# Kernel tuning notes

Measured on AMD Instinct MI355X. Metric: run time of the kernel, lower is better.

Reference implementation:

```python
import jax, jax.numpy as jnp
import numpy as np

NUM_LEAF = 10000   # leaf classes
BRANCH = 100       # leaves per parent node
NUM_PARENTS = NUM_LEAF // BRANCH  # 100 internal parent nodes (+ 1 implicit root)
BATCH = 4096


def setup_inputs() -> dict:
    key = jax.random.key(0)
    k1, k2 = jax.random.split(key)
    inp = jax.random.normal(k1, (BATCH, NUM_LEAF), dtype=jnp.float32)
    target = jax.random.randint(k2, (BATCH,), 0, NUM_LEAF)
    # structural tensor: parent id of each leaf in the 2-level taxonomy
    leaf_parent = (jnp.arange(NUM_LEAF) // BRANCH).astype(jnp.int32)
    return {"input": inp, "target": target, "leaf_parent": leaf_parent}


def _bce_to_one(p):
    # BCELoss(reduction='sum') against all-ones targets: -log(p), with torch's
    # log clamp at -100, after clipping p into [0, 1] as the module does.
    p = jnp.clip(p, 0.0, 1.0)
    return jnp.minimum(-jnp.log(p), 100.0)


def reference(input, target, leaf_parent):
    probs = jax.nn.softmax(input, axis=1)                       # [B, L]
    # mapping-sum for every internal parent node, all samples at once:
    # parent_probs[b, p] = sum_{l: parent(l)==p} probs[b, l]
    parent_probs = jax.ops.segment_sum(
        probs.T, leaf_parent, num_segments=NUM_PARENTS).T       # [B, P]
    b = jnp.arange(probs.shape[0])
    leaf_p = probs[b, target]                                   # group = leaf itself
    par_p = parent_probs[b, leaf_parent[target]]                # group = parent(leaf)
    root_p = probs.sum(axis=1)                                  # group = root (all leaves)
    per_sample = _bce_to_one(leaf_p) + _bce_to_one(par_p) + _bce_to_one(root_p)
    return per_sample.mean()  # reduction='mean'
```

## Files before the change

### kernel.cpp

```cpp
#include <hip/hip_runtime.h>


#define NUM_LEAF 10000
#define BRANCH   100
#define BATCH    4096
#define NV4      (NUM_LEAF / 4)

__global__ __launch_bounds__(256) void hce_row_kernel(
    const float* __restrict__ input,
    const int*   __restrict__ target,
    const int*   __restrict__ leaf_parent,
    float*       __restrict__ row_loss)
{
    const int row  = blockIdx.x;
    const int tid  = threadIdx.x;
    const int lane = tid & 63;
    const int wave = tid >> 6;

    const float*  x  = input + (size_t)row * NUM_LEAF;
    const float4* x4 = (const float4*)x;

    float s = 0.0f;
    for (int i = tid; i < NV4; i += 256) {
        float4 v = x4[i];
        s += __expf(v.x) + __expf(v.y) + __expf(v.z) + __expf(v.w);
    }
    #pragma unroll
    for (int off = 32; off; off >>= 1) s += __shfl_down(s, off, 64);

    __shared__ float wsum[4];
    __shared__ float Ssh;
    if (lane == 0) wsum[wave] = s;
    __syncthreads();
    if (tid == 0) Ssh = (wsum[0] + wsum[1]) + (wsum[2] + wsum[3]);
    __syncthreads();
    const float S = Ssh;

    if (wave == 0) {
        const int t = target[row];
        const int p = leaf_parent[t];
        float ps = 0.0f;
        if (lane < BRANCH / 4) {
            float4 v = x4[p * (BRANCH / 4) + lane];
            ps = __expf(v.x) + __expf(v.y) + __expf(v.z) + __expf(v.w);
        }
        #pragma unroll
        for (int off = 32; off; off >>= 1) ps += __shfl_down(ps, off, 64);

        if (lane == 0) {
            const float xt = x[t];
            const float lS = __logf(S);
            const float term_leaf = fminf(lS - xt,         100.0f);
            const float term_par  = fminf(lS - __logf(ps), 100.0f);
            row_loss[row] = term_leaf + term_par;
        }
    }
}

__global__ __launch_bounds__(256) void hce_reduce_kernel(
    const float* __restrict__ row_loss, float* __restrict__ out)
{
    const int tid = threadIdx.x;
    float s = 0.0f;
    for (int i = tid; i < BATCH; i += 256) s += row_loss[i];
    #pragma unroll
    for (int off = 32; off; off >>= 1) s += __shfl_down(s, off, 64);

    __shared__ float wsum[4];
    if ((tid & 63) == 0) wsum[tid >> 6] = s;
    __syncthreads();
    if (tid == 0) out[0] = ((wsum[0] + wsum[1]) + (wsum[2] + wsum[3])) * (1.0f / BATCH);
}

extern "C" void kernel_launch(void* const* d_in, const int* in_sizes, int n_in,
                              void* d_out, int out_size, void* d_ws, size_t ws_size,
                              hipStream_t stream) {
    const float* input       = (const float*)d_in[0];
    const int*   target      = (const int*)d_in[1];
    const int*   leaf_parent = (const int*)d_in[2];
    float*       out         = (float*)d_out;
    float*       row_loss    = (float*)d_ws;

    hce_row_kernel<<<BATCH, 256, 0, stream>>>(input, target, leaf_parent, row_loss);
    hce_reduce_kernel<<<1, 256, 0, stream>>>(row_loss, out);
}
```

Measured before the change: 34.81 us.

## Assign one wavefront per row to remove block-level barriers

```diff
diff --git a/kernel.cpp b/kernel.cpp
--- a/kernel.cpp
+++ b/kernel.cpp
@@ -5,6 +5,7 @@
 #define BRANCH   100
 #define BATCH    4096
 #define NV4      (NUM_LEAF / 4)
+#define WAVES_PER_BLOCK 4
 
 __global__ __launch_bounds__(256) void hce_row_kernel(
     const float* __restrict__ input,
@@ -12,48 +13,41 @@
     const int*   __restrict__ leaf_parent,
     float*       __restrict__ row_loss)
 {
-    const int row  = blockIdx.x;
-    const int tid  = threadIdx.x;
-    const int lane = tid & 63;
-    const int wave = tid >> 6;
+    const int lane = threadIdx.x & 63;
+    const int wave = threadIdx.x >> 6;
+    const int row  = blockIdx.x * WAVES_PER_BLOCK + wave;
 
     const float*  x  = input + (size_t)row * NUM_LEAF;
     const float4* x4 = (const float4*)x;
 
+    const int t  = target[row];
+    const int p  = leaf_parent[t];
+    const float xt = x[t];
+    float4 pv = make_float4(0.f, 0.f, 0.f, 0.f);
+    if (lane < BRANCH / 4)
+        pv = x4[p * (BRANCH / 4) + lane];
+
     float s = 0.0f;
-    for (int i = tid; i < NV4; i += 256) {
+    #pragma unroll 4
+    for (int i = lane; i < NV4; i += 64) {
         float4 v = x4[i];
         s += __expf(v.x) + __expf(v.y) + __expf(v.z) + __expf(v.w);
     }
     #pragma unroll
     for (int off = 32; off; off >>= 1) s += __shfl_down(s, off, 64);
+    const float S = __shfl(s, 0, 64);
 
-    __shared__ float wsum[4];
-    __shared__ float Ssh;
-    if (lane == 0) wsum[wave] = s;
-    __syncthreads();
-    if (tid == 0) Ssh = (wsum[0] + wsum[1]) + (wsum[2] + wsum[3]);
-    __syncthreads();
-    const float S = Ssh;
+    float ps = 0.0f;
+    if (lane < BRANCH / 4)
+        ps = __expf(pv.x) + __expf(pv.y) + __expf(pv.z) + __expf(pv.w);
+    #pragma unroll
+    for (int off = 32; off; off >>= 1) ps += __shfl_down(ps, off, 64);
 
-    if (wave == 0) {
-        const int t = target[row];
-        const int p = leaf_parent[t];
-        float ps = 0.0f;
-        if (lane < BRANCH / 4) {
-            float4 v = x4[p * (BRANCH / 4) + lane];
-            ps = __expf(v.x) + __expf(v.y) + __expf(v.z) + __expf(v.w);
-        }
-        #pragma unroll
-        for (int off = 32; off; off >>= 1) ps += __shfl_down(ps, off, 64);
-
-        if (lane == 0) {
-            const float xt = x[t];
-            const float lS = __logf(S);
-            const float term_leaf = fminf(lS - xt,         100.0f);
-            const float term_par  = fminf(lS - __logf(ps), 100.0f);
-            row_loss[row] = term_leaf + term_par;
-        }
+    if (lane == 0) {
+        const float lS = __logf(S);
+        const float term_leaf = fminf(lS - xt,         100.0f);
+        const float term_par  = fminf(lS - __logf(ps), 100.0f);
+        row_loss[row] = term_leaf + term_par;
     }
 }
 
@@ -81,6 +75,7 @@
     float*       out         = (float*)d_out;
     float*       row_loss    = (float*)d_ws;
 
-    hce_row_kernel<<<BATCH, 256, 0, stream>>>(input, target, leaf_parent, row_loss);
+    hce_row_kernel<<<BATCH / WAVES_PER_BLOCK, 256, 0, stream>>>(
+        input, target, leaf_parent, row_loss);
     hce_reduce_kernel<<<1, 256, 0, stream>>>(row_loss, out);
 }
```

Result: slower. 35.60 us (+2.2%).
